# Optimization experiments

Hardware: AMD Instinct MI355X
Metric: run time of the kernel (lower is better)

Reference implementation:

```python
import jax, jax.numpy as jnp
import numpy as np

B, T, V, D, H, K = 256, 128, 30000, 256, 256, 9  # H = hidden per direction (lstm_hidden//2)


def setup_inputs() -> dict:
    key = jax.random.key(0)
    ks = jax.random.split(key, 20)
    s = 0.05
    inp = {
        'input_x': jax.random.randint(ks[0], (B, T), 1, V),          # nonzero -> full mask
        'label':   jax.random.randint(ks[1], (B, T), 0, K),
        'emb':     jax.random.normal(ks[2], (V, D), jnp.float32) * 0.1,
        'Wih_f':   jax.random.normal(ks[3], (4 * H, D), jnp.float32) * s,
        'Whh_f':   jax.random.normal(ks[4], (4 * H, H), jnp.float32) * s,
        'b_f':     jnp.zeros((4 * H,), jnp.float32),
        'Wih_b':   jax.random.normal(ks[5], (4 * H, D), jnp.float32) * s,
        'Whh_b':   jax.random.normal(ks[6], (4 * H, H), jnp.float32) * s,
        'b_b':     jnp.zeros((4 * H,), jnp.float32),
        'W_emit':  jax.random.normal(ks[7], (K, 2 * H), jnp.float32) * s,
        'b_emit':  jnp.zeros((K,), jnp.float32),
        'start_t': jax.random.normal(ks[8], (K,), jnp.float32) * 0.1,
        'end_t':   jax.random.normal(ks[9], (K,), jnp.float32) * 0.1,
        'trans':   jax.random.normal(ks[10], (K, K), jnp.float32) * 0.1,
        'h0f':     jax.random.normal(ks[11], (B, H), jnp.float32),
        'c0f':     jax.random.normal(ks[12], (B, H), jnp.float32),
        'h0b':     jax.random.normal(ks[13], (B, H), jnp.float32),
        'c0b':     jax.random.normal(ks[14], (B, H), jnp.float32),
    }
    return inp


def _lstm_dir(x, h0, c0, Wih, Whh, b):
    # x: [B, T, D] -> outputs [B, T, H]; torch gate order i, f, g, o
    def step(carry, xt):
        h, c = carry
        g = xt @ Wih.T + h @ Whh.T + b
        i, f, gg, o = jnp.split(g, 4, axis=-1)
        c = jax.nn.sigmoid(f) * c + jax.nn.sigmoid(i) * jnp.tanh(gg)
        h = jax.nn.sigmoid(o) * jnp.tanh(c)
        return (h, c), h
    _, hs = jax.lax.scan(step, (h0, c0), jnp.swapaxes(x, 0, 1))
    return jnp.swapaxes(hs, 0, 1)


def _crf_loss(emis, tags, mask, start_t, end_t, trans):
    # torchcrf: -sum(log p(tags | emissions))
    mf = mask.astype(emis.dtype)
    bidx = jnp.arange(emis.shape[0])
    # numerator (gold path score)
    num = start_t[tags[:, 0]] + emis[bidx, 0, tags[:, 0]]
    num += jnp.sum(trans[tags[:, :-1], tags[:, 1:]] * mf[:, 1:], axis=1)
    emit_sc = jnp.take_along_axis(emis, tags[..., None], axis=-1)[..., 0]
    num += jnp.sum(emit_sc[:, 1:] * mf[:, 1:], axis=1)
    last_idx = jnp.sum(mask, axis=1) - 1
    num += end_t[tags[bidx, last_idx]]
    # denominator (log partition) via logsumexp recurrence
    def step(score, xs):
        emis_t, mask_t = xs  # [B,K], [B]
        nxt = jax.nn.logsumexp(score[:, :, None] + trans[None], axis=1) + emis_t
        score = jnp.where(mask_t[:, None], nxt, score)
        return score, None
    score0 = start_t + emis[:, 0]
    score, _ = jax.lax.scan(step, score0,
                            (jnp.swapaxes(emis[:, 1:], 0, 1), jnp.swapaxes(mask[:, 1:], 0, 1)))
    logZ = jax.nn.logsumexp(score + end_t, axis=-1)
    return -jnp.sum(num - logZ)


def _viterbi(emis, start_t, end_t, trans):
    # decode without mask (torchcrf decode(emissions)) -> [B, T] int tags
    def step(score, emis_t):
        tot = score[:, :, None] + trans[None]        # [B, K_prev, K_next]
        idx = jnp.argmax(tot, axis=1)                # [B, K]
        return jnp.max(tot, axis=1) + emis_t, idx
    score0 = start_t + emis[:, 0]
    score, hist = jax.lax.scan(step, score0, jnp.swapaxes(emis[:, 1:], 0, 1))  # hist [T-1,B,K]
    last = jnp.argmax(score + end_t, axis=-1)        # [B]
    def back(tag_next, h_t):
        tag = jnp.take_along_axis(h_t, tag_next[:, None], axis=1)[:, 0]
        return tag, tag
    _, tags_prev = jax.lax.scan(back, last, hist, reverse=True)  # [T-1, B]
    tags = jnp.concatenate([tags_prev, last[None]], axis=0)      # [T, B]
    return jnp.swapaxes(tags, 0, 1)


def reference(input_x, label, emb, Wih_f, Whh_f, b_f, Wih_b, Whh_b, b_b,
              W_emit, b_emit, start_t, end_t, trans, h0f, c0f, h0b, c0b):
    mask = input_x != 0
    x = emb[input_x]                                  # [B, T, D]
    hf = _lstm_dir(x, h0f, c0f, Wih_f, Whh_f, b_f)
    hb = _lstm_dir(x[:, ::-1], h0b, c0b, Wih_b, Whh_b, b_b)[:, ::-1]
    h = jnp.concatenate([hf, hb], axis=-1)            # [B, T, 2H]
    emis = h @ W_emit.T + b_emit                      # [B, T, K] (dropout = identity, eval)
    crf_loss = _crf_loss(emis, label, mask, start_t, end_t, trans)
    crf_decoder = _viterbi(emis, start_t, end_t, trans)
    return crf_loss, crf_decoder
```

## Files before the change

kernel.cpp:

```cpp
#include <hip/hip_runtime.h>

typedef __attribute__((ext_vector_type(8))) short bf16x8;
typedef __attribute__((ext_vector_type(4))) float f32x4;
typedef __attribute__((ext_vector_type(4))) unsigned u32x4;
typedef unsigned short u16;

#define SENT 0xC1C1C1C1u

__device__ __forceinline__ u16 f2bf(float f) {
  union { float f; unsigned u; } v; v.f = f;
  unsigned r = v.u + 0x7fffu + ((v.u >> 16) & 1u);
  return (u16)(r >> 16);
}
__device__ __forceinline__ unsigned cvt_pk(float lo, float hi) {
  unsigned r;
  asm("v_cvt_pk_bf16_f32 %0, %1, %2" : "=v"(r) : "v"(lo), "v"(hi));
  return r;
}
__device__ __forceinline__ float sigm(float x) { return 1.f / (1.f + __expf(-x)); }
__device__ __forceinline__ float tanhf_(float x) { return 1.f - 2.f / (__expf(2.f * x) + 1.f); }

__global__ __launch_bounds__(256) void k_prep(const float* __restrict__ emb,
    const float* __restrict__ wf, const float* __restrict__ wb, const float* __restrict__ we,
    char* __restrict__ eb8, char* __restrict__ wih8, u16* __restrict__ weh) {
  int i4 = (blockIdx.x * 256 + threadIdx.x) * 4;
  if (i4 < 8204288) {
    const float* src; char* dst; int o;
    if (i4 < 7680000) { src = emb + i4; dst = eb8; o = i4; }
    else { int off = i4 - 7680000;
           src = (off < 262144) ? (wf + off) : (wb + off - 262144);
           dst = wih8; o = off; }
    f32x4 v = *(const f32x4*)src;
    int r0 = __builtin_amdgcn_cvt_pk_fp8_f32(v[0], v[1], 0, false);
    r0 = __builtin_amdgcn_cvt_pk_fp8_f32(v[2], v[3], r0, true);
    *(int*)(dst + o) = r0;
  } else {
    int off = i4 - 8204288;
    int r = off >> 9, k = off & 511;
    f32x4 v = (r < 9) ? *(const f32x4*)(we + r * 512 + k) : (f32x4){0.f, 0.f, 0.f, 0.f};
    *(unsigned*)(weh + off) = cvt_pk(v[0], v[1]);
    *(unsigned*)(weh + off + 2) = cvt_pk(v[2], v[3]);
  }
}

#define LW 264
__global__ __launch_bounds__(256) void k_lstm(
    const float* __restrict__ whh_f, const float* __restrict__ whh_b,
    const char* __restrict__ wih8, const char* __restrict__ eb8,
    const int* __restrict__ ix,
    const float* __restrict__ bf_, const float* __restrict__ bb_,
    const float* __restrict__ h0f, const float* __restrict__ c0f,
    const float* __restrict__ h0b, const float* __restrict__ c0b,
    u16* __restrict__ hf, u16* __restrict__ hb) {
  __shared__ u16 wlh[128 * LW];
  __shared__ char wli8[128 * 264];
  __shared__ u16 hst[16 * LW];
  __shared__ __align__(16) char hsa8[16 * 272];
  __shared__ float gl[16 * 132];
  int bid = blockIdx.x;
  int js = (bid >> 3) & 7;
  int G = ((bid >> 6) << 3) | (bid & 7);
  int dir = G >> 4, bs = G & 15;
  const float* whh = dir ? whh_b : whh_f;
  u16* hout = dir ? hb : hf;
  int tid = threadIdx.x;
  for (int i = 0; i < 128; ++i) {
    int q = i >> 5, u = i & 31;
    int gate = q * 256 + js * 32 + u;
    wlh[i * LW + tid] = f2bf(whh[gate * 256 + tid]);
    wli8[i * 264 + tid] = wih8[(dir * 1024 + gate) * 256 + tid];
  }
  int b_l = tid >> 4, jj = tid & 15;
  int b_g = bs * 16 + b_l;
  int jg0 = js * 32 + jj * 2;
  const float* bsrc = dir ? bb_ : bf_;
  float bI0 = bsrc[jg0],       bI1 = bsrc[jg0 + 1];
  float bF0 = bsrc[256 + jg0], bF1 = bsrc[257 + jg0];
  float bG0 = bsrc[512 + jg0], bG1 = bsrc[513 + jg0];
  float bO0 = bsrc[768 + jg0], bO1 = bsrc[769 + jg0];
  const float* c0 = dir ? c0b : c0f;
  float cv0 = c0[b_g * 256 + jg0];
  float cv1 = c0[b_g * 256 + jg0 + 1];
  int w = tid >> 6, l = tid & 63, la = l & 15, lk = (l >> 4) * 8;
  int srow = tid >> 4, scol = (tid & 15) * 16;
  const float* h0 = dir ? h0b : h0f;
  const int* ixrow = ix + (bs * 16 + srow) * 128;
  u32x4 aR;
  {
    int tA = dir ? 127 : 0;
    const char* ap = eb8 + (long)ixrow[tA] * 256 + scol;
    aR = *(const u32x4*)ap;
  }
  __syncthreads();
  for (int sl = 0; sl < 128; ++sl) {
    int t_io = dir ? 127 - sl : sl;
    *(u32x4*)&hsa8[srow * 272 + scol] = aR;
    u16* hd = &hst[srow * LW + scol];
    if (sl == 0) {
      const float* p = h0 + (bs * 16 + srow) * 256 + scol;
      f32x4 v0 = *(const f32x4*)p, v1 = *(const f32x4*)(p + 4);
      f32x4 v2 = *(const f32x4*)(p + 8), v3 = *(const f32x4*)(p + 12);
      u32x4 qa, qb;
      qa[0] = cvt_pk(v0[0], v0[1]); qa[1] = cvt_pk(v0[2], v0[3]);
      qa[2] = cvt_pk(v1[0], v1[1]); qa[3] = cvt_pk(v1[2], v1[3]);
      qb[0] = cvt_pk(v2[0], v2[1]); qb[1] = cvt_pk(v2[2], v2[3]);
      qb[2] = cvt_pk(v3[0], v3[1]); qb[3] = cvt_pk(v3[2], v3[3]);
      *(u32x4*)hd = qa; *((u32x4*)hd + 1) = qb;
    } else {
      int tp = dir ? t_io + 1 : t_io - 1;
      const u16* p = hout + ((long)(bs * 16 + srow) * 128 + tp) * 256 + scol;
      u32x4 r0, r1; int guard = 0; bool ok;
      do {
        asm volatile(
          "global_load_dwordx4 %0, %2, off sc0 sc1\n\t"
          "global_load_dwordx4 %1, %2, off offset:16 sc0 sc1\n\t"
          "s_waitcnt vmcnt(0)"
          : "=v"(r0), "=v"(r1) : "v"(p) : "memory");
        ok = (r0[0] != SENT) & (r0[1] != SENT) & (r0[2] != SENT) & (r0[3] != SENT)
           & (r1[0] != SENT) & (r1[1] != SENT) & (r1[2] != SENT) & (r1[3] != SENT);
      } while (__builtin_expect(!ok, 0) && ++guard < (1 << 22));
      *(u32x4*)hd = r0; *((u32x4*)hd + 1) = r1;
    }
    __syncthreads();
    f32x4 a0 = (f32x4){0.f, 0.f, 0.f, 0.f}, a1 = (f32x4){0.f, 0.f, 0.f, 0.f};
#pragma unroll
    for (int ks = 0; ks < 8; ++ks) {
      int k = ks * 32 + lk;
      long xv = *(const long*)&hsa8[la * 272 + k];
      bf16x8 hh = *(const bf16x8*)&hst[la * LW + k];
      int r0_ = w * 32 + la, r1_ = w * 32 + 16 + la;
      long wi0 = *(const long*)&wli8[r0_ * 264 + k];
      long wi1 = *(const long*)&wli8[r1_ * 264 + k];
      bf16x8 wh0 = *(const bf16x8*)&wlh[r0_ * LW + k];
      bf16x8 wh1 = *(const bf16x8*)&wlh[r1_ * LW + k];
      a0 = __builtin_amdgcn_mfma_f32_16x16x32_fp8_fp8(xv, wi0, a0, 0, 0, 0);
      a0 = __builtin_amdgcn_mfma_f32_16x16x32_bf16(hh, wh0, a0, 0, 0, 0);
      a1 = __builtin_amdgcn_mfma_f32_16x16x32_fp8_fp8(xv, wi1, a1, 0, 0, 0);
      a1 = __builtin_amdgcn_mfma_f32_16x16x32_bf16(hh, wh1, a1, 0, 0, 0);
    }
#pragma unroll
    for (int r = 0; r < 4; ++r) {
      gl[((l >> 4) * 4 + r) * 132 + w * 32 + la] = a0[r];
      gl[((l >> 4) * 4 + r) * 132 + w * 32 + 16 + la] = a1[r];
    }
    __syncthreads();
    float hv0, hv1;
    {
      int jl = jj * 2;
      float gi = gl[b_l * 132 + jl]      + bI0;
      float gf = gl[b_l * 132 + 32 + jl] + bF0;
      float gg = gl[b_l * 132 + 64 + jl] + bG0;
      float go = gl[b_l * 132 + 96 + jl] + bO0;
      float c = sigm(gf) * cv0 + sigm(gi) * tanhf_(gg);
      cv0 = c; hv0 = sigm(go) * tanhf_(c);
    }
    {
      int jl = jj * 2 + 1;
      float gi = gl[b_l * 132 + jl]      + bI1;
      float gf = gl[b_l * 132 + 32 + jl] + bF1;
      float gg = gl[b_l * 132 + 64 + jl] + bG1;
      float go = gl[b_l * 132 + 96 + jl] + bO1;
      float c = sigm(gf) * cv1 + sigm(gi) * tanhf_(gg);
      cv1 = c; hv1 = sigm(go) * tanhf_(c);
    }
    unsigned pk = cvt_pk(hv0, hv1);
    __hip_atomic_store((unsigned*)(hout + ((long)b_g * 128 + t_io) * 256 + jg0), pk,
                       __ATOMIC_RELAXED, __HIP_MEMORY_SCOPE_AGENT);
    if (sl < 127) {
      int tN = dir ? 126 - sl : sl + 1;
      const char* ap = eb8 + (long)ixrow[tN] * 256 + scol;
      aR = *(const u32x4*)ap;
    }
  }
}

__global__ __launch_bounds__(256) void k_emis(const u16* __restrict__ hfb, const u16* __restrict__ hbb,
    const u16* __restrict__ weh, const float* __restrict__ bemit, float* __restrict__ emis,
    float* __restrict__ out) {
  if (blockIdx.x == 0 && threadIdx.x == 0) out[0] = 0.f;
  int w = threadIdx.x >> 6, l = threadIdx.x & 63;
  int la = l & 15, lk = (l >> 4) * 8;
  long m0 = (long)blockIdx.x * 64 + w * 16;
  long am = m0 + la;
  f32x4 acc = (f32x4){0.f, 0.f, 0.f, 0.f};
#pragma unroll
  for (int ks = 0; ks < 16; ++ks) {
    int k = ks * 32 + lk;
    const u16* src = (k < 256) ? (hfb + am * 256 + k) : (hbb + am * 256 + (k - 256));
    bf16x8 ah = *(const bf16x8*)src;
    bf16x8 bh = *(const bf16x8*)(weh + la * 512 + k);
    acc = __builtin_amdgcn_mfma_f32_16x16x32_bf16(ah, bh, acc, 0, 0, 0);
  }
  int kout = la;
  float bias = (kout < 9) ? bemit[kout] : 0.f;
  long mr = m0 + (l >> 4) * 4;
#pragma unroll
  for (int r = 0; r < 4; ++r)
    emis[(mr + r) * 16 + kout] = acc[r] + bias;
}

__global__ __launch_bounds__(256) void k_tail(const float* __restrict__ emis, const int* __restrict__ ixin,
    const int* __restrict__ label, const float* __restrict__ startt, const float* __restrict__ endt,
    const float* __restrict__ trans, float* __restrict__ out) {
  __shared__ float al_s[16][16];
  __shared__ float tr_s[9][16];
  __shared__ float num_s[16];
  __shared__ float red_s[16];
  __shared__ unsigned char bpl[16 * 127 * 16];
  int tid = threadIdx.x, bl = tid >> 4, k = tid & 15;
  int bid = blockIdx.x;
  if (bl < 9) tr_s[bl][k] = (k < 9) ? trans[bl * 9 + k] : 0.f;
  if (bid < 16) {
    int b = bid * 16 + bl;
    float a = 0.f, num = 0.f;
    int lastlab = 0;
    if (k < 9) a = startt[k] + emis[((long)b * 128) * 16 + k];
    al_s[bl][k] = a;
    if (k == 9) {
      int l0 = label[b * 128];
      num = startt[l0] + emis[((long)b * 128) * 16 + l0];
      lastlab = l0;
    }
    __syncthreads();
    for (int t = 1; t < 128; ++t) {
      bool msk = ixin[b * 128 + t] != 0;
      float anew = a;
      if (k < 9) {
        float mx = -1e30f;
#pragma unroll
        for (int j = 0; j < 9; ++j) mx = fmaxf(mx, al_s[bl][j] + tr_s[j][k]);
        float ss = 0.f;
#pragma unroll
        for (int j = 0; j < 9; ++j) ss += __expf(al_s[bl][j] + tr_s[j][k] - mx);
        anew = mx + __logf(ss) + emis[((long)b * 128 + t) * 16 + k];
        if (!msk) anew = a;
      } else if (k == 9 && msk) {
        int lt = label[b * 128 + t];
        num += tr_s[lastlab][lt] + emis[((long)b * 128 + t) * 16 + lt];
        lastlab = lt;
      }
      __syncthreads();
      if (k < 9) { a = anew; al_s[bl][k] = a; }
      __syncthreads();
    }
    if (k == 9) num_s[bl] = num + endt[lastlab];
    __syncthreads();
    if (k == 0) {
      float mx = -1e30f;
#pragma unroll
      for (int j = 0; j < 9; ++j) mx = fmaxf(mx, al_s[bl][j] + endt[j]);
      float ss = 0.f;
#pragma unroll
      for (int j = 0; j < 9; ++j) ss += __expf(al_s[bl][j] + endt[j] - mx);
      red_s[bl] = (mx + __logf(ss)) - num_s[bl];
    }
    __syncthreads();
    if (tid == 0) {
      float s = 0.f;
      for (int i = 0; i < 16; ++i) s += red_s[i];
      atomicAdd(out, s);
    }
  } else {
    int vb = bid - 16;
    int b = vb * 16 + bl;
    float v = -1e30f;
    if (k < 9) v = startt[k] + emis[((long)b * 128) * 16 + k];
    al_s[bl][k] = v;
    __syncthreads();
    for (int t = 1; t < 128; ++t) {
      float vnew = v;
      if (k < 9) {
        float best = -1e30f; int bi = 0;
#pragma unroll
        for (int j = 0; j < 9; ++j) {
          float tot = al_s[bl][j] + tr_s[j][k];
          if (tot > best) { best = tot; bi = j; }
        }
        vnew = best + emis[((long)b * 128 + t) * 16 + k];
        bpl[(bl * 127 + (t - 1)) * 16 + k] = (unsigned char)bi;
      }
      __syncthreads();
      if (k < 9) { v = vnew; al_s[bl][k] = v; }
      __syncthreads();
    }
    if (tid < 16) {
      int bb = vb * 16 + tid;
      float best = -1e30f; int tag = 0;
#pragma unroll
      for (int j = 0; j < 9; ++j) {
        float vv = al_s[tid][j] + endt[j];
        if (vv > best) { best = vv; tag = j; }
      }
      out[1 + bb * 128 + 127] = (float)tag;
      for (int t = 127; t >= 1; --t) {
        tag = bpl[(tid * 127 + (t - 1)) * 16 + tag];
        out[1 + bb * 128 + t - 1] = (float)tag;
      }
    }
  }
}

__global__ void k_sent(float* out) { out[0] = -1.0e6f; }

extern "C" void kernel_launch(void* const* d_in, const int* in_sizes, int n_in,
                              void* d_out, int out_size, void* d_ws, size_t ws_size,
                              hipStream_t stream) {
  const int* in_x    = (const int*)d_in[0];
  const int* label   = (const int*)d_in[1];
  const float* emb   = (const float*)d_in[2];
  const float* Wih_f = (const float*)d_in[3];
  const float* Whh_f = (const float*)d_in[4];
  const float* b_f   = (const float*)d_in[5];
  const float* Wih_b = (const float*)d_in[6];
  const float* Whh_b = (const float*)d_in[7];
  const float* b_b   = (const float*)d_in[8];
  const float* W_emit= (const float*)d_in[9];
  const float* b_emit= (const float*)d_in[10];
  const float* start_t=(const float*)d_in[11];
  const float* end_t = (const float*)d_in[12];
  const float* trans = (const float*)d_in[13];
  const float* h0f   = (const float*)d_in[14];
  const float* c0f   = (const float*)d_in[15];
  const float* h0b   = (const float*)d_in[16];
  const float* c0b   = (const float*)d_in[17];
  (void)in_sizes; (void)n_in; (void)out_size;

  auto align = [](size_t x) { return (x + 255) & ~(size_t)255; };
  char* ws = (char*)d_ws;
  size_t o = 0;
  auto alloc = [&](size_t sz) { size_t r = o; o += (sz + 255) & ~(size_t)255; return r; };
  size_t need = align(32768L * 256 * 2) * 2 + align(30000L * 256) + align(2048L * 256)
              + align(16L * 512 * 2) + align(32768L * 16 * 4);
  if (need > ws_size) { k_sent<<<1, 1, 0, stream>>>((float*)d_out); return; }

  u16* hf    = (u16*)(ws + alloc(32768L * 256 * 2));
  u16* hb    = (u16*)(ws + alloc(32768L * 256 * 2));
  char* eb8  = (char*)(ws + alloc(30000L * 256));
  char* wih8 = (char*)(ws + alloc(2048L * 256));
  u16* weh   = (u16*)(ws + alloc(16L * 512 * 2));
  float* emis= (float*)(ws + alloc(32768L * 16 * 4));

  hipMemsetAsync(hf, 0xC1, 32768L * 256 * 2, stream);
  hipMemsetAsync(hb, 0xC1, 32768L * 256 * 2, stream);
  k_prep<<<8020, 256, 0, stream>>>(emb, Wih_f, Wih_b, W_emit, eb8, wih8, weh);
  k_lstm<<<256, 256, 0, stream>>>(Whh_f, Whh_b, wih8, eb8, in_x, b_f, b_b,
                                  h0f, c0f, h0b, c0b, hf, hb);
  k_emis<<<512, 256, 0, stream>>>(hf, hb, weh, b_emit, emis, (float*)d_out);
  k_tail<<<32, 256, 0, stream>>>(emis, in_x, label, start_t, end_t, trans, (float*)d_out);
}
```

Measured before the change: 386.9 us.

## Quantize recurrent weights to fp8 and interleave two batch groups per LSTM block

Converts Whh to fp8 in the prep kernel and runs the recurrent matmul with fp8 MFMA instead of bf16, reading the previous hidden state as bf16 and requantizing it to fp8. The LSTM grid is halved to 128 blocks, and each block now handles two 16-row batch groups in alternating phases, so one group's global spin-wait on the previous hidden state can overlap the other group's compute. Weight staging into LDS now uses wider int loads. The cost is lower precision on the recurrent path and more serialized work per block.

```diff
diff --git a/kernel.cpp b/kernel.cpp
--- a/kernel.cpp
+++ b/kernel.cpp
@@ -7,22 +7,30 @@
 
 #define SENT 0xC1C1C1C1u
 
-__device__ __forceinline__ u16 f2bf(float f) {
-  union { float f; unsigned u; } v; v.f = f;
-  unsigned r = v.u + 0x7fffu + ((v.u >> 16) & 1u);
-  return (u16)(r >> 16);
-}
 __device__ __forceinline__ unsigned cvt_pk(float lo, float hi) {
   unsigned r;
   asm("v_cvt_pk_bf16_f32 %0, %1, %2" : "=v"(r) : "v"(lo), "v"(hi));
   return r;
 }
+__device__ __forceinline__ float bflo(unsigned d) { return __uint_as_float(d << 16); }
+__device__ __forceinline__ float bfhi(unsigned d) { return __uint_as_float(d & 0xffff0000u); }
 __device__ __forceinline__ float sigm(float x) { return 1.f / (1.f + __expf(-x)); }
 __device__ __forceinline__ float tanhf_(float x) { return 1.f - 2.f / (__expf(2.f * x) + 1.f); }
+__device__ __forceinline__ int pk4bf(unsigned w0, unsigned w1) {
+  int r = __builtin_amdgcn_cvt_pk_fp8_f32(bflo(w0), bfhi(w0), 0, false);
+  return __builtin_amdgcn_cvt_pk_fp8_f32(bflo(w1), bfhi(w1), r, true);
+}
+__device__ __forceinline__ int pk4f(float a, float b, float c, float d) {
+  int r = __builtin_amdgcn_cvt_pk_fp8_f32(a, b, 0, false);
+  return __builtin_amdgcn_cvt_pk_fp8_f32(c, d, r, true);
+}
 
 __global__ __launch_bounds__(256) void k_prep(const float* __restrict__ emb,
-    const float* __restrict__ wf, const float* __restrict__ wb, const float* __restrict__ we,
-    char* __restrict__ eb8, char* __restrict__ wih8, u16* __restrict__ weh) {
+    const float* __restrict__ wf, const float* __restrict__ wb,
+    const float* __restrict__ whf, const float* __restrict__ whb,
+    const float* __restrict__ we,
+    char* __restrict__ eb8, char* __restrict__ wih8, u16* __restrict__ weh,
+    char* __restrict__ whh8) {
   int i4 = (blockIdx.x * 256 + threadIdx.x) * 4;
   if (i4 < 8204288) {
     const float* src; char* dst; int o;
@@ -31,145 +39,229 @@
            src = (off < 262144) ? (wf + off) : (wb + off - 262144);
            dst = wih8; o = off; }
     f32x4 v = *(const f32x4*)src;
-    int r0 = __builtin_amdgcn_cvt_pk_fp8_f32(v[0], v[1], 0, false);
-    r0 = __builtin_amdgcn_cvt_pk_fp8_f32(v[2], v[3], r0, true);
-    *(int*)(dst + o) = r0;
-  } else {
+    *(int*)(dst + o) = pk4f(v[0], v[1], v[2], v[3]);
+  } else if (i4 < 8212480) {
     int off = i4 - 8204288;
     int r = off >> 9, k = off & 511;
     f32x4 v = (r < 9) ? *(const f32x4*)(we + r * 512 + k) : (f32x4){0.f, 0.f, 0.f, 0.f};
     *(unsigned*)(weh + off) = cvt_pk(v[0], v[1]);
     *(unsigned*)(weh + off + 2) = cvt_pk(v[2], v[3]);
+  } else {
+    int off = i4 - 8212480;
+    const float* src = (off < 262144) ? (whf + off) : (whb + off - 262144);
+    f32x4 v = *(const f32x4*)src;
+    *(int*)(whh8 + off) = pk4f(v[0], v[1], v[2], v[3]);
   }
 }
 
-#define LW 264
 __global__ __launch_bounds__(256) void k_lstm(
-    const float* __restrict__ whh_f, const float* __restrict__ whh_b,
-    const char* __restrict__ wih8, const char* __restrict__ eb8,
-    const int* __restrict__ ix,
+    const char* __restrict__ whh8, const char* __restrict__ wih8,
+    const char* __restrict__ eb8, const int* __restrict__ ix,
     const float* __restrict__ bf_, const float* __restrict__ bb_,
     const float* __restrict__ h0f, const float* __restrict__ c0f,
     const float* __restrict__ h0b, const float* __restrict__ c0b,
     u16* __restrict__ hf, u16* __restrict__ hb) {
-  __shared__ u16 wlh[128 * LW];
+  __shared__ char wlh8[128 * 264];
   __shared__ char wli8[128 * 264];
-  __shared__ u16 hst[16 * LW];
-  __shared__ __align__(16) char hsa8[16 * 272];
-  __shared__ float gl[16 * 132];
+  __shared__ __align__(16) char hs8[2][16 * 272];
+  __shared__ __align__(16) char xs8[2][16 * 272];
+  __shared__ float gl[2][16 * 132];
   int bid = blockIdx.x;
-  int js = (bid >> 3) & 7;
-  int G = ((bid >> 6) << 3) | (bid & 7);
-  int dir = G >> 4, bs = G & 15;
-  const float* whh = dir ? whh_b : whh_f;
+  int js = bid >> 4;
+  int rr = bid & 15;
+  int dir = rr >> 3, bsp = rr & 7;
   u16* hout = dir ? hb : hf;
   int tid = threadIdx.x;
-  for (int i = 0; i < 128; ++i) {
-    int q = i >> 5, u = i & 31;
-    int gate = q * 256 + js * 32 + u;
-    wlh[i * LW + tid] = f2bf(whh[gate * 256 + tid]);
-    wli8[i * 264 + tid] = wih8[(dir * 1024 + gate) * 256 + tid];
+#pragma unroll
+  for (int it = 0; it < 32; ++it) {
+    int idx = it * 256 + tid;
+    int row = idx >> 6, cd = (idx & 63) * 4;
+    int gate = (row >> 5) * 256 + js * 32 + (row & 31);
+    long go = (long)(dir * 1024 + gate) * 256 + cd;
+    *(int*)&wlh8[row * 264 + cd] = *(const int*)(whh8 + go);
+    *(int*)&wli8[row * 264 + cd] = *(const int*)(wih8 + go);
   }
   int b_l = tid >> 4, jj = tid & 15;
-  int b_g = bs * 16 + b_l;
   int jg0 = js * 32 + jj * 2;
+  int bgA = bsp * 32 + b_l, bgB = bgA + 16;
   const float* bsrc = dir ? bb_ : bf_;
   float bI0 = bsrc[jg0],       bI1 = bsrc[jg0 + 1];
   float bF0 = bsrc[256 + jg0], bF1 = bsrc[257 + jg0];
   float bG0 = bsrc[512 + jg0], bG1 = bsrc[513 + jg0];
   float bO0 = bsrc[768 + jg0], bO1 = bsrc[769 + jg0];
   const float* c0 = dir ? c0b : c0f;
-  float cv0 = c0[b_g * 256 + jg0];
-  float cv1 = c0[b_g * 256 + jg0 + 1];
+  float cvA0 = c0[bgA * 256 + jg0], cvA1 = c0[bgA * 256 + jg0 + 1];
+  float cvB0 = c0[bgB * 256 + jg0], cvB1 = c0[bgB * 256 + jg0 + 1];
   int w = tid >> 6, l = tid & 63, la = l & 15, lk = (l >> 4) * 8;
   int srow = tid >> 4, scol = (tid & 15) * 16;
+  int sgA = bsp * 32 + srow, sgB = sgA + 16;
   const float* h0 = dir ? h0b : h0f;
-  const int* ixrow = ix + (bs * 16 + srow) * 128;
-  u32x4 aR;
-  {
-    int tA = dir ? 127 : 0;
-    const char* ap = eb8 + (long)ixrow[tA] * 256 + scol;
-    aR = *(const u32x4*)ap;
-  }
+  const int* ixA = ix + sgA * 128;
+  const int* ixB = ix + sgB * 128;
+  int t0 = dir ? 127 : 0;
+  u32x4 aRA = *(const u32x4*)(eb8 + (long)ixA[t0] * 256 + scol);
+  u32x4 aRB = *(const u32x4*)(eb8 + (long)ixB[t0] * 256 + scol);
   __syncthreads();
   for (int sl = 0; sl < 128; ++sl) {
     int t_io = dir ? 127 - sl : sl;
-    *(u32x4*)&hsa8[srow * 272 + scol] = aR;
-    u16* hd = &hst[srow * LW + scol];
-    if (sl == 0) {
-      const float* p = h0 + (bs * 16 + srow) * 256 + scol;
-      f32x4 v0 = *(const f32x4*)p, v1 = *(const f32x4*)(p + 4);
-      f32x4 v2 = *(const f32x4*)(p + 8), v3 = *(const f32x4*)(p + 12);
-      u32x4 qa, qb;
-      qa[0] = cvt_pk(v0[0], v0[1]); qa[1] = cvt_pk(v0[2], v0[3]);
-      qa[2] = cvt_pk(v1[0], v1[1]); qa[3] = cvt_pk(v1[2], v1[3]);
-      qb[0] = cvt_pk(v2[0], v2[1]); qb[1] = cvt_pk(v2[2], v2[3]);
-      qb[2] = cvt_pk(v3[0], v3[1]); qb[3] = cvt_pk(v3[2], v3[3]);
-      *(u32x4*)hd = qa; *((u32x4*)hd + 1) = qb;
-    } else {
-      int tp = dir ? t_io + 1 : t_io - 1;
-      const u16* p = hout + ((long)(bs * 16 + srow) * 128 + tp) * 256 + scol;
-      u32x4 r0, r1; int guard = 0; bool ok;
-      do {
-        asm volatile(
-          "global_load_dwordx4 %0, %2, off sc0 sc1\n\t"
-          "global_load_dwordx4 %1, %2, off offset:16 sc0 sc1\n\t"
-          "s_waitcnt vmcnt(0)"
-          : "=v"(r0), "=v"(r1) : "v"(p) : "memory");
-        ok = (r0[0] != SENT) & (r0[1] != SENT) & (r0[2] != SENT) & (r0[3] != SENT)
-           & (r1[0] != SENT) & (r1[1] != SENT) & (r1[2] != SENT) & (r1[3] != SENT);
-      } while (__builtin_expect(!ok, 0) && ++guard < (1 << 22));
-      *(u32x4*)hd = r0; *((u32x4*)hd + 1) = r1;
-    }
-    __syncthreads();
-    f32x4 a0 = (f32x4){0.f, 0.f, 0.f, 0.f}, a1 = (f32x4){0.f, 0.f, 0.f, 0.f};
-#pragma unroll
-    for (int ks = 0; ks < 8; ++ks) {
-      int k = ks * 32 + lk;
-      long xv = *(const long*)&hsa8[la * 272 + k];
-      bf16x8 hh = *(const bf16x8*)&hst[la * LW + k];
-      int r0_ = w * 32 + la, r1_ = w * 32 + 16 + la;
-      long wi0 = *(const long*)&wli8[r0_ * 264 + k];
-      long wi1 = *(const long*)&wli8[r1_ * 264 + k];
-      bf16x8 wh0 = *(const bf16x8*)&wlh[r0_ * LW + k];
-      bf16x8 wh1 = *(const bf16x8*)&wlh[r1_ * LW + k];
-      a0 = __builtin_amdgcn_mfma_f32_16x16x32_fp8_fp8(xv, wi0, a0, 0, 0, 0);
-      a0 = __builtin_amdgcn_mfma_f32_16x16x32_bf16(hh, wh0, a0, 0, 0, 0);
-      a1 = __builtin_amdgcn_mfma_f32_16x16x32_fp8_fp8(xv, wi1, a1, 0, 0, 0);
-      a1 = __builtin_amdgcn_mfma_f32_16x16x32_bf16(hh, wh1, a1, 0, 0, 0);
-    }
-#pragma unroll
-    for (int r = 0; r < 4; ++r) {
-      gl[((l >> 4) * 4 + r) * 132 + w * 32 + la] = a0[r];
-      gl[((l >> 4) * 4 + r) * 132 + w * 32 + 16 + la] = a1[r];
-    }
-    __syncthreads();
-    float hv0, hv1;
-    {
-      int jl = jj * 2;
-      float gi = gl[b_l * 132 + jl]      + bI0;
-      float gf = gl[b_l * 132 + 32 + jl] + bF0;
-      float gg = gl[b_l * 132 + 64 + jl] + bG0;
-      float go = gl[b_l * 132 + 96 + jl] + bO0;
-      float c = sigm(gf) * cv0 + sigm(gi) * tanhf_(gg);
-      cv0 = c; hv0 = sigm(go) * tanhf_(c);
-    }
-    {
-      int jl = jj * 2 + 1;
-      float gi = gl[b_l * 132 + jl]      + bI1;
-      float gf = gl[b_l * 132 + 32 + jl] + bF1;
-      float gg = gl[b_l * 132 + 64 + jl] + bG1;
-      float go = gl[b_l * 132 + 96 + jl] + bO1;
-      float c = sigm(gf) * cv1 + sigm(gi) * tanhf_(gg);
-      cv1 = c; hv1 = sigm(go) * tanhf_(c);
-    }
-    unsigned pk = cvt_pk(hv0, hv1);
-    __hip_atomic_store((unsigned*)(hout + ((long)b_g * 128 + t_io) * 256 + jg0), pk,
-                       __ATOMIC_RELAXED, __HIP_MEMORY_SCOPE_AGENT);
-    if (sl < 127) {
-      int tN = dir ? 126 - sl : sl + 1;
-      const char* ap = eb8 + (long)ixrow[tN] * 256 + scol;
-      aR = *(const u32x4*)ap;
+    int tp = dir ? t_io + 1 : t_io - 1;
+    *(u32x4*)&xs8[0][srow * 272 + scol] = aRA;
+    {
+      int q0, q1, q2, q3;
+      if (sl == 0) {
+        const float* p = h0 + sgA * 256 + scol;
+        f32x4 v0 = *(const f32x4*)p, v1 = *(const f32x4*)(p + 4);
+        f32x4 v2 = *(const f32x4*)(p + 8), v3 = *(const f32x4*)(p + 12);
+        q0 = pk4f(v0[0], v0[1], v0[2], v0[3]); q1 = pk4f(v1[0], v1[1], v1[2], v1[3]);
+        q2 = pk4f(v2[0], v2[1], v2[2], v2[3]); q3 = pk4f(v3[0], v3[1], v3[2], v3[3]);
+      } else {
+        const u16* p = hout + ((long)sgA * 128 + tp) * 256 + scol;
+        u32x4 r0, r1; int guard = 0; bool ok;
+        do {
+          asm volatile(
+            "global_load_dwordx4 %0, %2, off sc0 sc1\n\t"
+            "global_load_dwordx4 %1, %2, off offset:16 sc0 sc1\n\t"
+            "s_waitcnt vmcnt(0)"
+            : "=v"(r0), "=v"(r1) : "v"(p) : "memory");
+          ok = (r0[0] != SENT) & (r0[1] != SENT) & (r0[2] != SENT) & (r0[3] != SENT)
+             & (r1[0] != SENT) & (r1[1] != SENT) & (r1[2] != SENT) & (r1[3] != SENT);
+        } while (__builtin_expect(!ok, 0) && ++guard < (1 << 22));
+        q0 = pk4bf(r0[0], r0[1]); q1 = pk4bf(r0[2], r0[3]);
+        q2 = pk4bf(r1[0], r1[1]); q3 = pk4bf(r1[2], r1[3]);
+      }
+      int4 qq = make_int4(q0, q1, q2, q3);
+      *(int4*)&hs8[0][srow * 272 + scol] = qq;
+    }
+    __syncthreads();
+    {
+      f32x4 a0 = (f32x4){0.f, 0.f, 0.f, 0.f}, a1 = (f32x4){0.f, 0.f, 0.f, 0.f};
+#pragma unroll
+      for (int ks = 0; ks < 8; ++ks) {
+        int k = ks * 32 + lk;
+        long xv = *(const long*)&xs8[0][la * 272 + k];
+        long hv = *(const long*)&hs8[0][la * 272 + k];
+        int r0_ = w * 32 + la, r1_ = r0_ + 16;
+        long wi0 = *(const long*)&wli8[r0_ * 264 + k];
+        long wh0 = *(const long*)&wlh8[r0_ * 264 + k];
+        long wi1 = *(const long*)&wli8[r1_ * 264 + k];
+        long wh1 = *(const long*)&wlh8[r1_ * 264 + k];
+        a0 = __builtin_amdgcn_mfma_f32_16x16x32_fp8_fp8(xv, wi0, a0, 0, 0, 0);
+        a0 = __builtin_amdgcn_mfma_f32_16x16x32_fp8_fp8(hv, wh0, a0, 0, 0, 0);
+        a1 = __builtin_amdgcn_mfma_f32_16x16x32_fp8_fp8(xv, wi1, a1, 0, 0, 0);
+        a1 = __builtin_amdgcn_mfma_f32_16x16x32_fp8_fp8(hv, wh1, a1, 0, 0, 0);
+      }
+#pragma unroll
+      for (int r = 0; r < 4; ++r) {
+        gl[0][((l >> 4) * 4 + r) * 132 + w * 32 + la] = a0[r];
+        gl[0][((l >> 4) * 4 + r) * 132 + w * 32 + 16 + la] = a1[r];
+      }
+    }
+    __syncthreads();
+    {
+      float hv0, hv1;
+      {
+        int jl = jj * 2;
+        float gi = gl[0][b_l * 132 + jl]      + bI0;
+        float gf = gl[0][b_l * 132 + 32 + jl] + bF0;
+        float gg = gl[0][b_l * 132 + 64 + jl] + bG0;
+        float go = gl[0][b_l * 132 + 96 + jl] + bO0;
+        float c = sigm(gf) * cvA0 + sigm(gi) * tanhf_(gg);
+        cvA0 = c; hv0 = sigm(go) * tanhf_(c);
+      }
+      {
+        int jl = jj * 2 + 1;
+        float gi = gl[0][b_l * 132 + jl]      + bI1;
+        float gf = gl[0][b_l * 132 + 32 + jl] + bF1;
+        float gg = gl[0][b_l * 132 + 64 + jl] + bG1;
+        float go = gl[0][b_l * 132 + 96 + jl] + bO1;
+        float c = sigm(gf) * cvA1 + sigm(gi) * tanhf_(gg);
+        cvA1 = c; hv1 = sigm(go) * tanhf_(c);
+      }
+      __hip_atomic_store((unsigned*)(hout + ((long)bgA * 128 + t_io) * 256 + jg0),
+                         cvt_pk(hv0, hv1), __ATOMIC_RELAXED, __HIP_MEMORY_SCOPE_AGENT);
+      if (sl < 127) {
+        int tN = dir ? 126 - sl : sl + 1;
+        aRA = *(const u32x4*)(eb8 + (long)ixA[tN] * 256 + scol);
+      }
+    }
+    *(u32x4*)&xs8[1][srow * 272 + scol] = aRB;
+    {
+      int q0, q1, q2, q3;
+      if (sl == 0) {
+        const float* p = h0 + sgB * 256 + scol;
+        f32x4 v0 = *(const f32x4*)p, v1 = *(const f32x4*)(p + 4);
+        f32x4 v2 = *(const f32x4*)(p + 8), v3 = *(const f32x4*)(p + 12);
+        q0 = pk4f(v0[0], v0[1], v0[2], v0[3]); q1 = pk4f(v1[0], v1[1], v1[2], v1[3]);
+        q2 = pk4f(v2[0], v2[1], v2[2], v2[3]); q3 = pk4f(v3[0], v3[1], v3[2], v3[3]);
+      } else {
+        const u16* p = hout + ((long)sgB * 128 + tp) * 256 + scol;
+        u32x4 r0, r1; int guard = 0; bool ok;
+        do {
+          asm volatile(
+            "global_load_dwordx4 %0, %2, off sc0 sc1\n\t"
+            "global_load_dwordx4 %1, %2, off offset:16 sc0 sc1\n\t"
+            "s_waitcnt vmcnt(0)"
+            : "=v"(r0), "=v"(r1) : "v"(p) : "memory");
+          ok = (r0[0] != SENT) & (r0[1] != SENT) & (r0[2] != SENT) & (r0[3] != SENT)
+             & (r1[0] != SENT) & (r1[1] != SENT) & (r1[2] != SENT) & (r1[3] != SENT);
+        } while (__builtin_expect(!ok, 0) && ++guard < (1 << 22));
+        q0 = pk4bf(r0[0], r0[1]); q1 = pk4bf(r0[2], r0[3]);
+        q2 = pk4bf(r1[0], r1[1]); q3 = pk4bf(r1[2], r1[3]);
+      }
+      int4 qq = make_int4(q0, q1, q2, q3);
+      *(int4*)&hs8[1][srow * 272 + scol] = qq;
+    }
+    __syncthreads();
+    {
+      f32x4 a0 = (f32x4){0.f, 0.f, 0.f, 0.f}, a1 = (f32x4){0.f, 0.f, 0.f, 0.f};
+#pragma unroll
+      for (int ks = 0; ks < 8; ++ks) {
+        int k = ks * 32 + lk;
+        long xv = *(const long*)&xs8[1][la * 272 + k];
+        long hv = *(const long*)&hs8[1][la * 272 + k];
+        int r0_ = w * 32 + la, r1_ = r0_ + 16;
+        long wi0 = *(const long*)&wli8[r0_ * 264 + k];
+        long wh0 = *(const long*)&wlh8[r0_ * 264 + k];
+        long wi1 = *(const long*)&wli8[r1_ * 264 + k];
+        long wh1 = *(const long*)&wlh8[r1_ * 264 + k];
+        a0 = __builtin_amdgcn_mfma_f32_16x16x32_fp8_fp8(xv, wi0, a0, 0, 0, 0);
+        a0 = __builtin_amdgcn_mfma_f32_16x16x32_fp8_fp8(hv, wh0, a0, 0, 0, 0);
+        a1 = __builtin_amdgcn_mfma_f32_16x16x32_fp8_fp8(xv, wi1, a1, 0, 0, 0);
+        a1 = __builtin_amdgcn_mfma_f32_16x16x32_fp8_fp8(hv, wh1, a1, 0, 0, 0);
+      }
+#pragma unroll
+      for (int r = 0; r < 4; ++r) {
+        gl[1][((l >> 4) * 4 + r) * 132 + w * 32 + la] = a0[r];
+        gl[1][((l >> 4) * 4 + r) * 132 + w * 32 + 16 + la] = a1[r];
+      }
+    }
+    __syncthreads();
+    {
+      float hv0, hv1;
+      {
+        int jl = jj * 2;
+        float gi = gl[1][b_l * 132 + jl]      + bI0;
+        float gf = gl[1][b_l * 132 + 32 + jl] + bF0;
+        float gg = gl[1][b_l * 132 + 64 + jl] + bG0;
+        float go = gl[1][b_l * 132 + 96 + jl] + bO0;
+        float c = sigm(gf) * cvB0 + sigm(gi) * tanhf_(gg);
+        cvB0 = c; hv0 = sigm(go) * tanhf_(c);
+      }
+      {
+        int jl = jj * 2 + 1;
+        float gi = gl[1][b_l * 132 + jl]      + bI1;
+        float gf = gl[1][b_l * 132 + 32 + jl] + bF1;
+        float gg = gl[1][b_l * 132 + 64 + jl] + bG1;
+        float go = gl[1][b_l * 132 + 96 + jl] + bO1;
+        float c = sigm(gf) * cvB1 + sigm(gi) * tanhf_(gg);
+        cvB1 = c; hv1 = sigm(go) * tanhf_(c);
+      }
+      __hip_atomic_store((unsigned*)(hout + ((long)bgB * 128 + t_io) * 256 + jg0),
+                         cvt_pk(hv0, hv1), __ATOMIC_RELAXED, __HIP_MEMORY_SCOPE_AGENT);
+      if (sl < 127) {
+        int tN = dir ? 126 - sl : sl + 1;
+        aRB = *(const u32x4*)(eb8 + (long)ixB[tN] * 256 + scol);
+      }
     }
   }
 }
@@ -329,7 +421,7 @@
   char* ws = (char*)d_ws;
   size_t o = 0;
   auto alloc = [&](size_t sz) { size_t r = o; o += (sz + 255) & ~(size_t)255; return r; };
-  size_t need = align(32768L * 256 * 2) * 2 + align(30000L * 256) + align(2048L * 256)
+  size_t need = align(32768L * 256 * 2) * 2 + align(30000L * 256) + align(2048L * 256) * 2
               + align(16L * 512 * 2) + align(32768L * 16 * 4);
   if (need > ws_size) { k_sent<<<1, 1, 0, stream>>>((float*)d_out); return; }
 
@@ -337,13 +429,15 @@
   u16* hb    = (u16*)(ws + alloc(32768L * 256 * 2));
   char* eb8  = (char*)(ws + alloc(30000L * 256));
   char* wih8 = (char*)(ws + alloc(2048L * 256));
+  char* whh8 = (char*)(ws + alloc(2048L * 256));
   u16* weh   = (u16*)(ws + alloc(16L * 512 * 2));
   float* emis= (float*)(ws + alloc(32768L * 16 * 4));
 
   hipMemsetAsync(hf, 0xC1, 32768L * 256 * 2, stream);
   hipMemsetAsync(hb, 0xC1, 32768L * 256 * 2, stream);
-  k_prep<<<8020, 256, 0, stream>>>(emb, Wih_f, Wih_b, W_emit, eb8, wih8, weh);
-  k_lstm<<<256, 256, 0, stream>>>(Whh_f, Whh_b, wih8, eb8, in_x, b_f, b_b,
+  k_prep<<<8532, 256, 0, stream>>>(emb, Wih_f, Wih_b, Whh_f, Whh_b, W_emit,
+                                   eb8, wih8, weh, whh8);
+  k_lstm<<<128, 256, 0, stream>>>(whh8, wih8, eb8, in_x, b_f, b_b,
                                   h0f, c0f, h0b, c0b, hf, hb);
   k_emis<<<512, 256, 0, stream>>>(hf, hb, weh, b_emit, emis, (float*)d_out);
   k_tail<<<32, 256, 0, stream>>>(emis, in_x, label, start_t, end_t, trans, (float*)d_out);
```

Result: slower. 606.3 us (+56.7%).

## Interleave gate rows so MFMA outputs feed LSTM cell directly, drop gate LDS round-trip

Applied to the files above, without the earlier changes.

Reorders the recurrent and input weight rows so each MFMA output lane holds the i,f,g,o gates of one hidden unit, and swaps MFMA operand order so the cell update runs directly from accumulators. This removes the gate scratch buffer in shared memory and one barrier per timestep. Embedding fragments are loaded straight into registers instead of staged through LDS, and the h state buffer is double-buffered so the second barrier is no longer needed. Outputs become 16-bit stores with the sentinel check done per half-word, which adds more store instructions and puts more weight on cross-block visibility ordering.

```diff
diff --git a/kernel.cpp b/kernel.cpp
--- a/kernel.cpp
+++ b/kernel.cpp
@@ -5,7 +5,7 @@
 typedef __attribute__((ext_vector_type(4))) unsigned u32x4;
 typedef unsigned short u16;
 
-#define SENT 0xC1C1C1C1u
+#define SENT16 0xC1C1u
 
 __device__ __forceinline__ u16 f2bf(float f) {
   union { float f; unsigned u; } v; v.f = f;
@@ -19,6 +19,13 @@
 }
 __device__ __forceinline__ float sigm(float x) { return 1.f / (1.f + __expf(-x)); }
 __device__ __forceinline__ float tanhf_(float x) { return 1.f - 2.f / (__expf(2.f * x) + 1.f); }
+__device__ __forceinline__ int pk4f(float a, float b, float c, float d) {
+  int r = __builtin_amdgcn_cvt_pk_fp8_f32(a, b, 0, false);
+  return __builtin_amdgcn_cvt_pk_fp8_f32(c, d, r, true);
+}
+__device__ __forceinline__ bool half_ok(unsigned v) {
+  return ((v & 0xFFFFu) != SENT16) & ((v >> 16) != SENT16);
+}
 
 __global__ __launch_bounds__(256) void k_prep(const float* __restrict__ emb,
     const float* __restrict__ wf, const float* __restrict__ wb, const float* __restrict__ we,
@@ -31,9 +38,7 @@
            src = (off < 262144) ? (wf + off) : (wb + off - 262144);
            dst = wih8; o = off; }
     f32x4 v = *(const f32x4*)src;
-    int r0 = __builtin_amdgcn_cvt_pk_fp8_f32(v[0], v[1], 0, false);
-    r0 = __builtin_amdgcn_cvt_pk_fp8_f32(v[2], v[3], r0, true);
-    *(int*)(dst + o) = r0;
+    *(int*)(dst + o) = pk4f(v[0], v[1], v[2], v[3]);
   } else {
     int off = i4 - 8204288;
     int r = off >> 9, k = off & 511;
@@ -54,9 +59,7 @@
     u16* __restrict__ hf, u16* __restrict__ hb) {
   __shared__ u16 wlh[128 * LW];
   __shared__ char wli8[128 * 264];
-  __shared__ u16 hst[16 * LW];
-  __shared__ __align__(16) char hsa8[16 * 272];
-  __shared__ float gl[16 * 132];
+  __shared__ u16 hst[2][16 * LW];
   int bid = blockIdx.x;
   int js = (bid >> 3) & 7;
   int G = ((bid >> 6) << 3) | (bid & 7);
@@ -65,37 +68,36 @@
   u16* hout = dir ? hb : hf;
   int tid = threadIdx.x;
   for (int i = 0; i < 128; ++i) {
-    int q = i >> 5, u = i & 31;
-    int gate = q * 256 + js * 32 + u;
+    int jl = i >> 2, q = i & 3;
+    int gate = q * 256 + js * 32 + jl;
     wlh[i * LW + tid] = f2bf(whh[gate * 256 + tid]);
     wli8[i * 264 + tid] = wih8[(dir * 1024 + gate) * 256 + tid];
   }
-  int b_l = tid >> 4, jj = tid & 15;
-  int b_g = bs * 16 + b_l;
-  int jg0 = js * 32 + jj * 2;
+  int w = tid >> 6, l = tid & 63;
+  int lb = l & 15, lk8 = (l >> 4) * 8;
+  int b_g = bs * 16 + lb;
+  int j0 = js * 32 + w * 8 + (l >> 4);
+  int j1 = j0 + 4;
   const float* bsrc = dir ? bb_ : bf_;
-  float bI0 = bsrc[jg0],       bI1 = bsrc[jg0 + 1];
-  float bF0 = bsrc[256 + jg0], bF1 = bsrc[257 + jg0];
-  float bG0 = bsrc[512 + jg0], bG1 = bsrc[513 + jg0];
-  float bO0 = bsrc[768 + jg0], bO1 = bsrc[769 + jg0];
+  f32x4 bv0 = { bsrc[j0], bsrc[256 + j0], bsrc[512 + j0], bsrc[768 + j0] };
+  f32x4 bv1 = { bsrc[j1], bsrc[256 + j1], bsrc[512 + j1], bsrc[768 + j1] };
   const float* c0 = dir ? c0b : c0f;
-  float cv0 = c0[b_g * 256 + jg0];
-  float cv1 = c0[b_g * 256 + jg0 + 1];
-  int w = tid >> 6, l = tid & 63, la = l & 15, lk = (l >> 4) * 8;
+  float cv0 = c0[b_g * 256 + j0];
+  float cv1 = c0[b_g * 256 + j1];
   int srow = tid >> 4, scol = (tid & 15) * 16;
   const float* h0 = dir ? h0b : h0f;
-  const int* ixrow = ix + (bs * 16 + srow) * 128;
-  u32x4 aR;
+  long xb[8];
   {
-    int tA = dir ? 127 : 0;
-    const char* ap = eb8 + (long)ixrow[tA] * 256 + scol;
-    aR = *(const u32x4*)ap;
+    int t0 = dir ? 127 : 0;
+    long xrow = (long)ix[b_g * 128 + t0] * 256;
+#pragma unroll
+    for (int ks = 0; ks < 8; ++ks) xb[ks] = *(const long*)(eb8 + xrow + ks * 32 + lk8);
   }
   __syncthreads();
+  int cur = 0;
   for (int sl = 0; sl < 128; ++sl) {
     int t_io = dir ? 127 - sl : sl;
-    *(u32x4*)&hsa8[srow * 272 + scol] = aR;
-    u16* hd = &hst[srow * LW + scol];
+    u16* hd = &hst[cur][srow * LW + scol];
     if (sl == 0) {
       const float* p = h0 + (bs * 16 + srow) * 256 + scol;
       f32x4 v0 = *(const f32x4*)p, v1 = *(const f32x4*)(p + 4);
@@ -116,61 +118,52 @@
           "global_load_dwordx4 %1, %2, off offset:16 sc0 sc1\n\t"
           "s_waitcnt vmcnt(0)"
           : "=v"(r0), "=v"(r1) : "v"(p) : "memory");
-        ok = (r0[0] != SENT) & (r0[1] != SENT) & (r0[2] != SENT) & (r0[3] != SENT)
-           & (r1[0] != SENT) & (r1[1] != SENT) & (r1[2] != SENT) & (r1[3] != SENT);
+        ok = half_ok(r0[0]) & half_ok(r0[1]) & half_ok(r0[2]) & half_ok(r0[3])
+           & half_ok(r1[0]) & half_ok(r1[1]) & half_ok(r1[2]) & half_ok(r1[3]);
       } while (__builtin_expect(!ok, 0) && ++guard < (1 << 22));
       *(u32x4*)hd = r0; *((u32x4*)hd + 1) = r1;
     }
     __syncthreads();
-    f32x4 a0 = (f32x4){0.f, 0.f, 0.f, 0.f}, a1 = (f32x4){0.f, 0.f, 0.f, 0.f};
+    bf16x8 hbf[8];
+#pragma unroll
+    for (int ks = 0; ks < 8; ++ks)
+      hbf[ks] = *(const bf16x8*)&hst[cur][lb * LW + ks * 32 + lk8];
+    f32x4 acc0 = bv0, acc1 = bv1;
 #pragma unroll
     for (int ks = 0; ks < 8; ++ks) {
-      int k = ks * 32 + lk;
-      long xv = *(const long*)&hsa8[la * 272 + k];
-      bf16x8 hh = *(const bf16x8*)&hst[la * LW + k];
-      int r0_ = w * 32 + la, r1_ = w * 32 + 16 + la;
+      int k = ks * 32 + lk8;
+      int r0_ = w * 32 + lb, r1_ = r0_ + 16;
       long wi0 = *(const long*)&wli8[r0_ * 264 + k];
       long wi1 = *(const long*)&wli8[r1_ * 264 + k];
       bf16x8 wh0 = *(const bf16x8*)&wlh[r0_ * LW + k];
       bf16x8 wh1 = *(const bf16x8*)&wlh[r1_ * LW + k];
-      a0 = __builtin_amdgcn_mfma_f32_16x16x32_fp8_fp8(xv, wi0, a0, 0, 0, 0);
-      a0 = __builtin_amdgcn_mfma_f32_16x16x32_bf16(hh, wh0, a0, 0, 0, 0);
-      a1 = __builtin_amdgcn_mfma_f32_16x16x32_fp8_fp8(xv, wi1, a1, 0, 0, 0);
-      a1 = __builtin_amdgcn_mfma_f32_16x16x32_bf16(hh, wh1, a1, 0, 0, 0);
-    }
-#pragma unroll
-    for (int r = 0; r < 4; ++r) {
-      gl[((l >> 4) * 4 + r) * 132 + w * 32 + la] = a0[r];
-      gl[((l >> 4) * 4 + r) * 132 + w * 32 + 16 + la] = a1[r];
-    }
-    __syncthreads();
-    float hv0, hv1;
+      acc0 = __builtin_amdgcn_mfma_f32_16x16x32_fp8_fp8(wi0, xb[ks], acc0, 0, 0, 0);
+      acc0 = __builtin_amdgcn_mfma_f32_16x16x32_bf16(wh0, hbf[ks], acc0, 0, 0, 0);
+      acc1 = __builtin_amdgcn_mfma_f32_16x16x32_fp8_fp8(wi1, xb[ks], acc1, 0, 0, 0);
+      acc1 = __builtin_amdgcn_mfma_f32_16x16x32_bf16(wh1, hbf[ks], acc1, 0, 0, 0);
+    }
+    long hrow = ((long)b_g * 128 + t_io) * 256;
     {
-      int jl = jj * 2;
-      float gi = gl[b_l * 132 + jl]      + bI0;
-      float gf = gl[b_l * 132 + 32 + jl] + bF0;
-      float gg = gl[b_l * 132 + 64 + jl] + bG0;
-      float go = gl[b_l * 132 + 96 + jl] + bO0;
-      float c = sigm(gf) * cv0 + sigm(gi) * tanhf_(gg);
-      cv0 = c; hv0 = sigm(go) * tanhf_(c);
+      float c = sigm(acc0[1]) * cv0 + sigm(acc0[0]) * tanhf_(acc0[2]);
+      cv0 = c;
+      u16 hv = f2bf(sigm(acc0[3]) * tanhf_(c));
+      asm volatile("global_store_short %0, %1, off sc0 sc1"
+                   :: "v"(hout + hrow + j0), "v"((unsigned)hv) : "memory");
     }
     {
-      int jl = jj * 2 + 1;
-      float gi = gl[b_l * 132 + jl]      + bI1;
-      float gf = gl[b_l * 132 + 32 + jl] + bF1;
-      float gg = gl[b_l * 132 + 64 + jl] + bG1;
-      float go = gl[b_l * 132 + 96 + jl] + bO1;
-      float c = sigm(gf) * cv1 + sigm(gi) * tanhf_(gg);
-      cv1 = c; hv1 = sigm(go) * tanhf_(c);
-    }
-    unsigned pk = cvt_pk(hv0, hv1);
-    __hip_atomic_store((unsigned*)(hout + ((long)b_g * 128 + t_io) * 256 + jg0), pk,
-                       __ATOMIC_RELAXED, __HIP_MEMORY_SCOPE_AGENT);
+      float c = sigm(acc1[1]) * cv1 + sigm(acc1[0]) * tanhf_(acc1[2]);
+      cv1 = c;
+      u16 hv = f2bf(sigm(acc1[3]) * tanhf_(c));
+      asm volatile("global_store_short %0, %1, off sc0 sc1"
+                   :: "v"(hout + hrow + j1), "v"((unsigned)hv) : "memory");
+    }
     if (sl < 127) {
       int tN = dir ? 126 - sl : sl + 1;
-      const char* ap = eb8 + (long)ixrow[tN] * 256 + scol;
-      aR = *(const u32x4*)ap;
-    }
+      long xrow = (long)ix[b_g * 128 + tN] * 256;
+#pragma unroll
+      for (int ks = 0; ks < 8; ++ks) xb[ks] = *(const long*)(eb8 + xrow + ks * 32 + lk8);
+    }
+    cur ^= 1;
   }
 }
 
```

New measurement: 580.9 us. +50.1%, slower.
